# Kernel optimization log

Measured on AMD Instinct MI355X. Metric: run time of the kernel, lower is better.

Reference implementation:

```python
import jax, jax.numpy as jnp
import numpy as np

ANCHORS = jnp.array([[0.57273, 0.677385], [1.87446, 2.06253], [3.33843, 5.47434],
                     [7.88282, 3.52778], [9.77052, 9.16828]], dtype=jnp.float32)
IOU_THR = 0.6
SCALE_NOOBJ = 1.0
SCALE_OBJ = 5.0
DS = 32.0          # downsample_rate
EPS = 1e-7


def _iou_wh(w1, h1, w2, h2):
    # GetCenterAlignIouBetween: boxes aligned at centers -> IoU depends on w,h only
    inter = jnp.minimum(w1, w2) * jnp.minimum(h1, h2)
    return inter / (w1 * h1 + w2 * h2 - inter + EPS)


def setup_inputs() -> dict:
    B, W, H, A, C, M = 128, 19, 19, 5, 81, 24
    N = W * H
    key = jax.random.key(0)
    ks = jax.random.split(key, 8)
    ii, jj = jnp.meshgrid(jnp.arange(W), jnp.arange(H), indexing='ij')
    fm_cord = jnp.stack([jj, ii], -1).reshape(N, 2).astype(jnp.float32)  # (x=j, y=i)
    conf = jax.random.uniform(ks[0], (B, W, H, A, 1)) * 0.98 + 0.01      # valid BCE probs
    pred_xy = fm_cord.reshape(1, W, H, 1, 2) + jax.random.uniform(ks[1], (B, W, H, A, 2))
    pred_wh = jax.random.uniform(ks[2], (B, W, H, A, 2)) * 8.0 + 0.2     # fm units, >0
    cls_score = jax.random.normal(ks[3], (B, W, H, A, C))
    # distinct grid cells per image so sequential scatter == vectorized scatter
    cells = jax.vmap(lambda k: jax.random.choice(k, N, (M,), replace=False))(
        jax.random.split(ks[4], B))
    ci = cells // H
    cj = cells % H
    frac = jax.random.uniform(ks[5], (B, M, 2))
    x = (cj.astype(jnp.float32) + frac[..., 0]) * DS   # pixel coords
    y = (ci.astype(jnp.float32) + frac[..., 1]) * DS
    wh = jax.random.uniform(ks[6], (B, M, 2), minval=12.0, maxval=280.0)
    true_object = jnp.stack([x, y, wh[..., 0], wh[..., 1]], -1)          # [B,M,4] pixels
    labels = jax.random.randint(ks[7], (B, M), 0, C - 1)
    true_label = jax.nn.one_hot(labels, C, dtype=jnp.float32)            # [B,M,C]
    return dict(epoch=0, conf=conf, pred_xy=pred_xy, pred_wh=pred_wh,
                cls_score=cls_score, true_label=true_label,
                true_object=true_object, fm_cord=fm_cord)


def _yolo_loss(conf, pred_xy, pred_wh, cls_score, true_label, true_object, fm_cord):
    B, W, H, A, C = cls_score.shape
    N = W * H
    NA = N * A
    S = float(W)  # config.output_size

    # ---- target assignment (vectorized version of the python loops) ----
    obj = true_object / DS                               # fm units, [B,M,4]
    gx, gy, gw, gh = obj[..., 0], obj[..., 1], obj[..., 2], obj[..., 3]
    i = gy.astype(jnp.int32)                             # row index  (int() truncation)
    j = gx.astype(jnp.int32)                             # col index
    cell = i * H + j                                     # flat cell, [B,M]

    a_iou = _iou_wh(ANCHORS[None, None, :, 0], ANCHORS[None, None, :, 1],
                    gw[..., None], gh[..., None])        # [B,M,A]
    best = jnp.argmax(a_iou, axis=-1)                    # [B,M]
    is_best = best[..., None] == jnp.arange(A)[None, None, :]
    over = a_iou > IOU_THR

    bb = jnp.arange(B)[:, None]
    pwh = pred_wh.reshape(B, N, A, 2)[bb, cell]          # [B,M,A,2] gather at gt cells
    pwh_b = jnp.take_along_axis(pwh, best[..., None, None], axis=2)[:, :, 0]  # [B,M,2]
    iou_pg = _iou_wh(pwh_b[..., 0], pwh_b[..., 1], gw, gh)                    # [B,M]

    mask_val = jnp.where(is_best, 1.0, jnp.where(over, -1.0, 0.0))            # [B,M,A]
    sw = 2.0 - (gw / S) * (gh / S)                                            # [B,M]
    sw_val = jnp.where(is_best, sw[..., None], jnp.where(over, -1.0, 0.0))
    pgi_val = jnp.where(~is_best & over, 0.0, iou_pg[..., None])              # [B,M,A]
    bg = jax.nn.one_hot(C - 1, C, dtype=cls_score.dtype)
    ts_val = jnp.where((is_best | over)[..., None], true_label[:, :, None, :], bg)
    bbox_val = jnp.where(is_best[..., None], obj[:, :, None, :], 0.0)         # [B,M,A,4]

    obj_mask = jnp.zeros((B, N, A)).at[bb, cell].set(mask_val)
    scale_w = jnp.zeros((B, N, A)).at[bb, cell].set(sw_val)
    pgi = jnp.zeros((B, N, A)).at[bb, cell].set(pgi_val)
    true_score = jnp.zeros((B, N, A, C)).at[..., -1].set(1.0).at[bb, cell].set(ts_val)
    true_bbox = jnp.zeros((B, N, A, 4)).at[bb, cell].set(bbox_val)

    # ---- masked losses over flattened [B, W*H*A, ...] ----
    conf_f = conf.reshape(B, NA)
    om = obj_mask.reshape(B, NA)
    swf = scale_w.reshape(B, NA)
    pgif = pgi.reshape(B, NA)
    pxy = pred_xy.reshape(B, NA, 2)
    pwh_f = pred_wh.reshape(B, NA, 2)
    tb = true_bbox.reshape(B, NA, 4)
    ts = true_score.reshape(B, NA, C)
    cs = cls_score.reshape(B, NA, C)
    cord = jnp.repeat(fm_cord[:, None, :], A, axis=1).reshape(NA, 2)

    cp = jnp.clip(conf_f, EPS, 1.0 - EPS)
    noobj_loss = SCALE_NOOBJ * jnp.sum((om == 0) * (-jnp.log(1.0 - cp))) / B
    obj_loss = SCALE_OBJ * jnp.sum(
        (om == 1) * (-(pgif * jnp.log(cp) + (1.0 - pgif) * jnp.log(1.0 - cp)))) / B

    gt = (swf > 0).astype(conf_f.dtype)                  # [B,NA]
    w3 = (SCALE_OBJ * gt * swf)[..., None]
    xy_loss = jnp.sum(w3 * ((pxy - cord[None]) - (tb[..., :2] - cord[None])) ** 2) / B
    wh_loss = jnp.sum(w3 * (pwh_f - tb[..., 2:]) ** 2) / B

    # CE with soft targets, per position: [B,NA]
    ce = -jnp.sum(ts * jax.nn.log_softmax(cs, axis=-1), axis=-1)
    # original broadcasts mask [B,1,NA] * ce [B,NA] -> [B,B,NA] then .sum();
    # equivalent factored form: sum_n (sum_b1 mask) * (sum_b2 ce)
    score_loss = SCALE_OBJ * jnp.sum(gt.sum(0) * ce.sum(0)) / B

    total = noobj_loss + obj_loss + xy_loss + wh_loss + score_loss
    return total, noobj_loss, obj_loss, score_loss, xy_loss, wh_loss


def reference(epoch, conf, pred_xy, pred_wh, cls_score, true_label, true_object, fm_cord):
    return _yolo_loss(conf, pred_xy, pred_wh, cls_score,
                      true_label, true_object, fm_cord)
```

## Files before the change

kernel.cpp:

```cpp
#include <hip/hip_runtime.h>

#define Bsz 128
#define Wd 19
#define Hd 19
#define Ad 5
#define Cd 81
#define Md 24
#define Nd (Wd*Hd)
#define NAd (Nd*Ad)
#define TOTPOS (Bsz*NAd)
#define PPB 128
#define EPSF 1e-7f
#define IOU_THRF 0.6f

#define WS_FLOATS (4 + 2*NAd)

__global__ __launch_bounds__(64) void yolo_assign(
        const float* __restrict__ conf,
        const float* __restrict__ pred_xy,
        const float* __restrict__ pred_wh,
        const float* __restrict__ cls_score,
        const float* __restrict__ true_label,
        const float* __restrict__ true_object,
        float* __restrict__ ws) {
    int idx = blockIdx.x * 64 + threadIdx.x;
    const float AW[5] = {0.57273f, 1.87446f, 3.33843f, 7.88282f, 9.77052f};
    const float AH[5] = {0.677385f, 2.06253f, 5.47434f, 3.52778f, 9.16828f};
    int b = idx / Md;

    const float4 to = ((const float4*)true_object)[idx];
    const float inv_ds = 1.0f / 32.0f;
    float gx = to.x * inv_ds, gy = to.y * inv_ds;
    float gw = to.z * inv_ds, gh = to.w * inv_ds;
    int ci = (int)gy, cj = (int)gx;
    int cell = ci * Hd + cj;
    float garea = gw * gh;

    float best_iou = -1.0f; int best = 0; bool over[Ad];
    #pragma unroll
    for (int a = 0; a < Ad; a++) {
        float inter = fminf(AW[a], gw) * fminf(AH[a], gh);
        float iou = inter / (AW[a] * AH[a] + garea - inter + EPSF);
        over[a] = iou > IOU_THRF;
        if (iou > best_iou) { best_iou = iou; best = a; }
    }

    const float* tl = true_label + (size_t)idx * Cd;
    float labf = 0.0f;
    for (int c = 0; c < Cd; c++) labf += tl[c] * (float)c;
    int lab = (int)(labf + 0.5f);

    int base_bn = (b * Nd + cell) * Ad;
    float pwb = pred_wh[(size_t)(base_bn + best) * 2 + 0];
    float phb = pred_wh[(size_t)(base_bn + best) * 2 + 1];
    float inter = fminf(pwb, gw) * fminf(phb, gh);
    float iou_pg = inter / (pwb * phb + garea - inter + EPSF);
    float sw = 2.0f - (gw * (1.0f / 19.0f)) * (gh * (1.0f / 19.0f));

    float* gtsum = ws + 4;
    float* cesum = ws + 4 + NAd;

    float a0 = 0.f, a1 = 0.f, a2 = 0.f, a3 = 0.f;
    #pragma unroll
    for (int a = 0; a < Ad; a++) {
        bool isb = (a == best);
        if (!(isb || over[a])) continue;
        int pos = base_bn + a;
        int na  = cell * Ad + a;
        float cp = fminf(fmaxf(conf[pos], EPSF), 1.0f - EPSF);
        a0 += __logf(1.0f - cp);
        const float* cs = cls_score + (size_t)pos * Cd;
        atomicAdd(&cesum[na], cs[Cd - 1] - cs[lab]);
        if (isb) {
            atomicAdd(&gtsum[na], 1.0f);
            a1 += -(iou_pg * __logf(cp) + (1.0f - iou_pg) * __logf(1.0f - cp));
            float px = pred_xy[(size_t)pos * 2 + 0], py = pred_xy[(size_t)pos * 2 + 1];
            a2 += sw * ((px - gx) * (px - gx) + (py - gy) * (py - gy));
            float pwa = pred_wh[(size_t)pos * 2 + 0], pha = pred_wh[(size_t)pos * 2 + 1];
            a3 += sw * ((pwa - gw) * (pwa - gw) + (pha - gh) * (pha - gh));
        }
    }

    #pragma unroll
    for (int off = 32; off > 0; off >>= 1) {
        a0 += __shfl_down(a0, off, 64);
        a1 += __shfl_down(a1, off, 64);
        a2 += __shfl_down(a2, off, 64);
        a3 += __shfl_down(a3, off, 64);
    }
    if (threadIdx.x == 0) {
        atomicAdd(&ws[0], a0);
        atomicAdd(&ws[1], a1);
        atomicAdd(&ws[2], a2);
        atomicAdd(&ws[3], a3);
    }
}

__global__ __launch_bounds__(256) void yolo_sweep(
        const float* __restrict__ conf,
        const float* __restrict__ cls_score,
        float* __restrict__ ws) {
    __shared__ float ex[PPB * Cd];
    __shared__ float red[4];
    const int tid = threadIdx.x;
    const int bid = blockIdx.x;
    const int CHUNK4 = PPB * Cd / 4;

    const float4* g = (const float4*)(cls_score + (size_t)bid * (PPB * Cd));
    float4* l4 = (float4*)ex;
    for (int k = tid; k < CHUNK4; k += 256) {
        float4 v = g[k];
        v.x = __expf(v.x); v.y = __expf(v.y);
        v.z = __expf(v.z); v.w = __expf(v.w);
        l4[k] = v;
    }

    float noobj = 0.0f;
    if (tid < PPB) {
        float cp = fminf(fmaxf(conf[bid * PPB + tid], EPSF), 1.0f - EPSF);
        noobj = -__logf(1.0f - cp);
    }
    __syncthreads();

    int pos = tid >> 1, half = tid & 1;
    const float* base = ex + pos * Cd;
    float s = 0.0f;
    int c0 = half * 40, c1 = half ? Cd : 40;
    for (int c = c0; c < c1; c++) s += base[c];
    float S = s + __shfl_xor(s, 1, 64);
    if (half == 0) {
        float ce = __logf(S) - __logf(base[Cd - 1]);
        int na = (bid * PPB) % NAd + pos;
        if (na >= NAd) na -= NAd;
        atomicAdd(&ws[4 + NAd + na], ce);
    }

    #pragma unroll
    for (int off = 32; off > 0; off >>= 1) noobj += __shfl_down(noobj, off, 64);
    if ((tid & 63) == 0) red[tid >> 6] = noobj;
    __syncthreads();
    if (tid == 0) atomicAdd(&ws[0], red[0] + red[1] + red[2] + red[3]);
}

__global__ void yolo_finalize(const float* __restrict__ ws, float* __restrict__ out) {
    __shared__ float red[4];
    const float* gtsum = ws + 4;
    const float* cesum = ws + 4 + NAd;
    float s = 0.0f;
    for (int na = threadIdx.x; na < NAd; na += blockDim.x)
        s += gtsum[na] * cesum[na];
    #pragma unroll
    for (int off = 32; off > 0; off >>= 1) s += __shfl_down(s, off, 64);
    if ((threadIdx.x & 63) == 0) red[threadIdx.x >> 6] = s;
    __syncthreads();
    if (threadIdx.x == 0) {
        float tot = red[0] + red[1] + red[2] + red[3];
        const float invB = 1.0f / (float)Bsz;
        float noobj = 1.0f * ws[0] * invB;
        float obj   = 5.0f * ws[1] * invB;
        float xy    = 5.0f * ws[2] * invB;
        float wh    = 5.0f * ws[3] * invB;
        float score = 5.0f * tot  * invB;
        out[0] = noobj + obj + xy + wh + score;
        out[1] = noobj;
        out[2] = obj;
        out[3] = score;
        out[4] = xy;
        out[5] = wh;
    }
}

extern "C" void kernel_launch(void* const* d_in, const int* in_sizes, int n_in,
                              void* d_out, int out_size, void* d_ws, size_t ws_size,
                              hipStream_t stream) {
    const float* conf    = (const float*)d_in[1];
    const float* pred_xy = (const float*)d_in[2];
    const float* pred_wh = (const float*)d_in[3];
    const float* cls     = (const float*)d_in[4];
    const float* tlabel  = (const float*)d_in[5];
    const float* tobject = (const float*)d_in[6];
    float* ws  = (float*)d_ws;
    float* out = (float*)d_out;

    hipMemsetAsync(ws, 0, WS_FLOATS * sizeof(float), stream);

    yolo_assign<<<48, 64, 0, stream>>>(conf, pred_xy, pred_wh, cls, tlabel, tobject, ws);

    yolo_sweep<<<TOTPOS / PPB, 256, 0, stream>>>(conf, cls, ws);

    yolo_finalize<<<1, 256, 0, stream>>>(ws, out);
}
```

Before: 159.4 us.

## Replace per-position CE atomics with plain stores and reduce columns in finalize

The sweep kernel now handles 64 positions per block with four threads per position and applies exp while summing, instead of exponentiating during the shared-memory staging. It writes each per-position cross-entropy to its own workspace slot rather than issuing an atomicAdd into a per-anchor array. The finalize kernel, widened to 1024 threads, sums those values over the batch for each anchor slot. The assign kernel reads each label vector with a whole wavefront and runs after the sweep. Atomic contention goes away, but the workspace grows by one float per position and a single block must reduce all of them.

```diff
diff --git a/kernel.cpp b/kernel.cpp
--- a/kernel.cpp
+++ b/kernel.cpp
@@ -9,13 +9,16 @@
 #define Nd (Wd*Hd)
 #define NAd (Nd*Ad)
 #define TOTPOS (Bsz*NAd)
-#define PPB 128
+#define PPB 64
 #define EPSF 1e-7f
 #define IOU_THRF 0.6f
 
-#define WS_FLOATS (4 + 2*NAd)
-
-__global__ __launch_bounds__(64) void yolo_assign(
+#define OFF_GT   4
+#define OFF_CORR (4 + NAd)
+#define OFF_CE   4096
+#define MEMSET_FLOATS (4 + 2*NAd)
+
+__global__ __launch_bounds__(256) void yolo_assign(
         const float* __restrict__ conf,
         const float* __restrict__ pred_xy,
         const float* __restrict__ pred_wh,
@@ -23,76 +26,79 @@
         const float* __restrict__ true_label,
         const float* __restrict__ true_object,
         float* __restrict__ ws) {
-    int idx = blockIdx.x * 64 + threadIdx.x;
     const float AW[5] = {0.57273f, 1.87446f, 3.33843f, 7.88282f, 9.77052f};
     const float AH[5] = {0.677385f, 2.06253f, 5.47434f, 3.52778f, 9.16828f};
-    int b = idx / Md;
-
-    const float4 to = ((const float4*)true_object)[idx];
-    const float inv_ds = 1.0f / 32.0f;
-    float gx = to.x * inv_ds, gy = to.y * inv_ds;
-    float gw = to.z * inv_ds, gh = to.w * inv_ds;
-    int ci = (int)gy, cj = (int)gx;
-    int cell = ci * Hd + cj;
-    float garea = gw * gh;
-
-    float best_iou = -1.0f; int best = 0; bool over[Ad];
-    #pragma unroll
-    for (int a = 0; a < Ad; a++) {
-        float inter = fminf(AW[a], gw) * fminf(AH[a], gh);
-        float iou = inter / (AW[a] * AH[a] + garea - inter + EPSF);
-        over[a] = iou > IOU_THRF;
-        if (iou > best_iou) { best_iou = iou; best = a; }
-    }
-
-    const float* tl = true_label + (size_t)idx * Cd;
-    float labf = 0.0f;
-    for (int c = 0; c < Cd; c++) labf += tl[c] * (float)c;
-    int lab = (int)(labf + 0.5f);
-
-    int base_bn = (b * Nd + cell) * Ad;
-    float pwb = pred_wh[(size_t)(base_bn + best) * 2 + 0];
-    float phb = pred_wh[(size_t)(base_bn + best) * 2 + 1];
-    float inter = fminf(pwb, gw) * fminf(phb, gh);
-    float iou_pg = inter / (pwb * phb + garea - inter + EPSF);
-    float sw = 2.0f - (gw * (1.0f / 19.0f)) * (gh * (1.0f / 19.0f));
-
-    float* gtsum = ws + 4;
-    float* cesum = ws + 4 + NAd;
-
+    int wave = threadIdx.x >> 6, lane = threadIdx.x & 63;
     float a0 = 0.f, a1 = 0.f, a2 = 0.f, a3 = 0.f;
-    #pragma unroll
-    for (int a = 0; a < Ad; a++) {
-        bool isb = (a == best);
-        if (!(isb || over[a])) continue;
-        int pos = base_bn + a;
-        int na  = cell * Ad + a;
-        float cp = fminf(fmaxf(conf[pos], EPSF), 1.0f - EPSF);
-        a0 += __logf(1.0f - cp);
-        const float* cs = cls_score + (size_t)pos * Cd;
-        atomicAdd(&cesum[na], cs[Cd - 1] - cs[lab]);
-        if (isb) {
-            atomicAdd(&gtsum[na], 1.0f);
-            a1 += -(iou_pg * __logf(cp) + (1.0f - iou_pg) * __logf(1.0f - cp));
-            float px = pred_xy[(size_t)pos * 2 + 0], py = pred_xy[(size_t)pos * 2 + 1];
-            a2 += sw * ((px - gx) * (px - gx) + (py - gy) * (py - gy));
-            float pwa = pred_wh[(size_t)pos * 2 + 0], pha = pred_wh[(size_t)pos * 2 + 1];
-            a3 += sw * ((pwa - gw) * (pwa - gw) + (pha - gh) * (pha - gh));
+    float* gtsum = ws + OFF_GT;
+    float* corr  = ws + OFF_CORR;
+
+    int objBase = (blockIdx.x * 4 + wave) * 8;
+    for (int o = 0; o < 8; o++) {
+        int idx = objBase + o;
+        const float* tl = true_label + (size_t)idx * Cd;
+        float labf = tl[lane] * (float)lane;
+        if (lane < Cd - 64) labf += tl[64 + lane] * (float)(64 + lane);
+        #pragma unroll
+        for (int off = 32; off > 0; off >>= 1) labf += __shfl_down(labf, off, 64);
+
+        if (lane == 0) {
+            int lab = (int)(labf + 0.5f);
+            int b = idx / Md;
+            const float4 to = ((const float4*)true_object)[idx];
+            const float inv_ds = 1.0f / 32.0f;
+            float gx = to.x * inv_ds, gy = to.y * inv_ds;
+            float gw = to.z * inv_ds, gh = to.w * inv_ds;
+            int ci = (int)gy, cj = (int)gx;
+            int cell = ci * Hd + cj;
+            float garea = gw * gh;
+
+            float best_iou = -1.0f; int best = 0; bool over[Ad];
+            #pragma unroll
+            for (int a = 0; a < Ad; a++) {
+                float inter = fminf(AW[a], gw) * fminf(AH[a], gh);
+                float iou = inter / (AW[a] * AH[a] + garea - inter + EPSF);
+                over[a] = iou > IOU_THRF;
+                if (iou > best_iou) { best_iou = iou; best = a; }
+            }
+
+            int base_bn = (b * Nd + cell) * Ad;
+            float pwb = pred_wh[(size_t)(base_bn + best) * 2 + 0];
+            float phb = pred_wh[(size_t)(base_bn + best) * 2 + 1];
+            float inter = fminf(pwb, gw) * fminf(phb, gh);
+            float iou_pg = inter / (pwb * phb + garea - inter + EPSF);
+            float sw = 2.0f - (gw * (1.0f / 19.0f)) * (gh * (1.0f / 19.0f));
+
+            #pragma unroll
+            for (int a = 0; a < Ad; a++) {
+                bool isb = (a == best);
+                if (!(isb || over[a])) continue;
+                int pos = base_bn + a;
+                int na  = cell * Ad + a;
+                float cp = fminf(fmaxf(conf[pos], EPSF), 1.0f - EPSF);
+                a0 += __logf(1.0f - cp);
+                const float* cs = cls_score + (size_t)pos * Cd;
+                atomicAdd(&corr[na], cs[Cd - 1] - cs[lab]);
+                if (isb) {
+                    atomicAdd(&gtsum[na], 1.0f);
+                    a1 += -(iou_pg * __logf(cp) + (1.0f - iou_pg) * __logf(1.0f - cp));
+                    float px = pred_xy[(size_t)pos * 2 + 0], py = pred_xy[(size_t)pos * 2 + 1];
+                    a2 += sw * ((px - gx) * (px - gx) + (py - gy) * (py - gy));
+                    float pwa = pred_wh[(size_t)pos * 2 + 0], pha = pred_wh[(size_t)pos * 2 + 1];
+                    a3 += sw * ((pwa - gw) * (pwa - gw) + (pha - gh) * (pha - gh));
+                }
+            }
         }
     }
 
-    #pragma unroll
-    for (int off = 32; off > 0; off >>= 1) {
-        a0 += __shfl_down(a0, off, 64);
-        a1 += __shfl_down(a1, off, 64);
-        a2 += __shfl_down(a2, off, 64);
-        a3 += __shfl_down(a3, off, 64);
-    }
+    __shared__ float red[4][4];
+    if (lane == 0) { red[wave][0] = a0; red[wave][1] = a1; red[wave][2] = a2; red[wave][3] = a3; }
+    __syncthreads();
     if (threadIdx.x == 0) {
-        atomicAdd(&ws[0], a0);
-        atomicAdd(&ws[1], a1);
-        atomicAdd(&ws[2], a2);
-        atomicAdd(&ws[3], a3);
+        atomicAdd(&ws[0], red[0][0] + red[1][0] + red[2][0] + red[3][0]);
+        atomicAdd(&ws[1], red[0][1] + red[1][1] + red[2][1] + red[3][1]);
+        atomicAdd(&ws[2], red[0][2] + red[1][2] + red[2][2] + red[3][2]);
+        atomicAdd(&ws[3], red[0][3] + red[1][3] + red[2][3] + red[3][3]);
     }
 }
 
@@ -101,60 +107,75 @@
         const float* __restrict__ cls_score,
         float* __restrict__ ws) {
     __shared__ float ex[PPB * Cd];
-    __shared__ float red[4];
-    const int tid = threadIdx.x;
-    const int bid = blockIdx.x;
-    const int CHUNK4 = PPB * Cd / 4;
+    const int tid = threadIdx.x, bid = blockIdx.x;
+    const int wave = tid >> 6, lane = tid & 63;
+    const int base = wave * 324;
 
     const float4* g = (const float4*)(cls_score + (size_t)bid * (PPB * Cd));
     float4* l4 = (float4*)ex;
-    for (int k = tid; k < CHUNK4; k += 256) {
-        float4 v = g[k];
-        v.x = __expf(v.x); v.y = __expf(v.y);
-        v.z = __expf(v.z); v.w = __expf(v.w);
-        l4[k] = v;
-    }
-
-    float noobj = 0.0f;
+
+    float4 r0 = g[base + 0 * 64 + lane];
+    float4 r1 = g[base + 1 * 64 + lane];
+    float4 r2 = g[base + 2 * 64 + lane];
+    float4 r3 = g[base + 3 * 64 + lane];
+    float4 r4 = g[base + 4 * 64 + lane];
+    float4 r5 = g[base + 260 + lane];
+
+    float nb = 0.0f;
     if (tid < PPB) {
         float cp = fminf(fmaxf(conf[bid * PPB + tid], EPSF), 1.0f - EPSF);
-        noobj = -__logf(1.0f - cp);
-    }
+        nb = -__logf(1.0f - cp);
+    }
+
+    l4[base + 0 * 64 + lane] = r0;
+    l4[base + 1 * 64 + lane] = r1;
+    l4[base + 2 * 64 + lane] = r2;
+    l4[base + 3 * 64 + lane] = r3;
+    l4[base + 4 * 64 + lane] = r4;
+    l4[base + 260 + lane] = r5;
     __syncthreads();
 
-    int pos = tid >> 1, half = tid & 1;
-    const float* base = ex + pos * Cd;
+    int pos = tid >> 2, h = tid & 3;
+    const float* p = ex + pos * Cd;
+    int c0 = h * 20, c1 = (h == 3) ? Cd : c0 + 20;
     float s = 0.0f;
-    int c0 = half * 40, c1 = half ? Cd : 40;
-    for (int c = c0; c < c1; c++) s += base[c];
-    float S = s + __shfl_xor(s, 1, 64);
-    if (half == 0) {
-        float ce = __logf(S) - __logf(base[Cd - 1]);
-        int na = (bid * PPB) % NAd + pos;
-        if (na >= NAd) na -= NAd;
-        atomicAdd(&ws[4 + NAd + na], ce);
-    }
-
-    #pragma unroll
-    for (int off = 32; off > 0; off >>= 1) noobj += __shfl_down(noobj, off, 64);
-    if ((tid & 63) == 0) red[tid >> 6] = noobj;
-    __syncthreads();
-    if (tid == 0) atomicAdd(&ws[0], red[0] + red[1] + red[2] + red[3]);
-}
-
-__global__ void yolo_finalize(const float* __restrict__ ws, float* __restrict__ out) {
-    __shared__ float red[4];
-    const float* gtsum = ws + 4;
-    const float* cesum = ws + 4 + NAd;
+    for (int c = c0; c < c1; c++) s += __expf(p[c]);
+    s += __shfl_xor(s, 1, 64);
+    s += __shfl_xor(s, 2, 64);
+    if (h == 0) {
+        float ce = __logf(s) - p[Cd - 1];
+        ws[OFF_CE + bid * PPB + pos] = ce;
+    }
+
+    if (wave == 0) {
+        #pragma unroll
+        for (int off = 32; off > 0; off >>= 1) nb += __shfl_down(nb, off, 64);
+        if (lane == 0) atomicAdd(&ws[0], nb);
+    }
+}
+
+__global__ __launch_bounds__(1024) void yolo_finalize(
+        const float* __restrict__ ws, float* __restrict__ out) {
+    __shared__ float red[16];
+    const float* gtsum = ws + OFF_GT;
+    const float* corr  = ws + OFF_CORR;
+    const float* cef   = ws + OFF_CE;
     float s = 0.0f;
-    for (int na = threadIdx.x; na < NAd; na += blockDim.x)
-        s += gtsum[na] * cesum[na];
+    for (int na = threadIdx.x; na < NAd; na += 1024) {
+        float sum = corr[na];
+        const float* col = cef + na;
+        #pragma unroll 4
+        for (int b = 0; b < Bsz; b++) sum += col[(size_t)b * NAd];
+        s += gtsum[na] * sum;
+    }
     #pragma unroll
     for (int off = 32; off > 0; off >>= 1) s += __shfl_down(s, off, 64);
     if ((threadIdx.x & 63) == 0) red[threadIdx.x >> 6] = s;
     __syncthreads();
     if (threadIdx.x == 0) {
-        float tot = red[0] + red[1] + red[2] + red[3];
+        float tot = 0.f;
+        #pragma unroll
+        for (int i = 0; i < 16; i++) tot += red[i];
         const float invB = 1.0f / (float)Bsz;
         float noobj = 1.0f * ws[0] * invB;
         float obj   = 5.0f * ws[1] * invB;
@@ -182,11 +203,11 @@
     float* ws  = (float*)d_ws;
     float* out = (float*)d_out;
 
-    hipMemsetAsync(ws, 0, WS_FLOATS * sizeof(float), stream);
-
-    yolo_assign<<<48, 64, 0, stream>>>(conf, pred_xy, pred_wh, cls, tlabel, tobject, ws);
+    hipMemsetAsync(ws, 0, MEMSET_FLOATS * sizeof(float), stream);
 
     yolo_sweep<<<TOTPOS / PPB, 256, 0, stream>>>(conf, cls, ws);
 
-    yolo_finalize<<<1, 256, 0, stream>>>(ws, out);
-}
+    yolo_assign<<<96, 256, 0, stream>>>(conf, pred_xy, pred_wh, cls, tlabel, tobject, ws);
+
+    yolo_finalize<<<1, 1024, 0, stream>>>(ws, out);
+}
```

New measurement: 210.3 us. 31.9% more time.

## Merge assignment into sweep and final kernels with per-wave row blocks

Applied to the files above, without the earlier changes.

Removes the separate assignment kernel. Label decoding moves into the sweep kernel as extra one-wave blocks, and the target-assignment work moves into a single 1024-thread final kernel that accumulates into shared-memory atomics. The sweep now launches one 64-lane block per 16 rows, so many more blocks share the load, and each block writes its no-object partial to its own slot instead of issuing global atomics. The cost is that assignment runs serially inside one block at the end, which could become the critical path.

```diff
diff --git a/kernel.cpp b/kernel.cpp
--- a/kernel.cpp
+++ b/kernel.cpp
@@ -1,166 +1,194 @@
 #include <hip/hip_runtime.h>
 
 #define Bsz 128
-#define Wd 19
-#define Hd 19
-#define Ad 5
 #define Cd 81
 #define Md 24
-#define Nd (Wd*Hd)
-#define NAd (Nd*Ad)
-#define TOTPOS (Bsz*NAd)
-#define PPB 128
+#define Nd 361
+#define NAd 1805
+#define TOTPOS 231040
+#define RPW 16
+#define NW_CLS (TOTPOS/RPW)
+#define NOBJ (Bsz*Md)
+#define NW_LAB (NOBJ/RPW)
 #define EPSF 1e-7f
 #define IOU_THRF 0.6f
 
-#define WS_FLOATS (4 + 2*NAd)
-
-__global__ __launch_bounds__(64) void yolo_assign(
+#define OFF_CESUM 0
+#define OFF_NOOBJ 2048
+#define OFF_LAB   17408
+
+__global__ __launch_bounds__(64) void yolo_sweep(
+        const float* __restrict__ conf,
+        const float* __restrict__ cls_score,
+        const float* __restrict__ true_label,
+        float* __restrict__ ws) {
+    __shared__ float ex[RPW * Cd];
+    const int bid = blockIdx.x;
+    const int lane = threadIdx.x;
+    const bool is_cls = bid < NW_CLS;
+
+    const float* src = is_cls ? (cls_score + (size_t)bid * (RPW * Cd))
+                              : (true_label + (size_t)(bid - NW_CLS) * (RPW * Cd));
+    const float4* g = (const float4*)src;
+    float4 r0 = g[0 * 64 + lane];
+    float4 r1 = g[1 * 64 + lane];
+    float4 r2 = g[2 * 64 + lane];
+    float4 r3 = g[3 * 64 + lane];
+    float4 r4 = g[4 * 64 + lane];
+    float4 r5 = g[260 + lane];
+
+    float nb = 0.0f;
+    if (is_cls) {
+        if (lane < RPW) {
+            float cp = fminf(fmaxf(conf[bid * RPW + lane], EPSF), 1.0f - EPSF);
+            nb = -__logf(1.0f - cp);
+        }
+        r0.x = __expf(r0.x); r0.y = __expf(r0.y); r0.z = __expf(r0.z); r0.w = __expf(r0.w);
+        r1.x = __expf(r1.x); r1.y = __expf(r1.y); r1.z = __expf(r1.z); r1.w = __expf(r1.w);
+        r2.x = __expf(r2.x); r2.y = __expf(r2.y); r2.z = __expf(r2.z); r2.w = __expf(r2.w);
+        r3.x = __expf(r3.x); r3.y = __expf(r3.y); r3.z = __expf(r3.z); r3.w = __expf(r3.w);
+        r4.x = __expf(r4.x); r4.y = __expf(r4.y); r4.z = __expf(r4.z); r4.w = __expf(r4.w);
+        r5.x = __expf(r5.x); r5.y = __expf(r5.y); r5.z = __expf(r5.z); r5.w = __expf(r5.w);
+    }
+    float4* l4 = (float4*)ex;
+    l4[0 * 64 + lane] = r0;
+    l4[1 * 64 + lane] = r1;
+    l4[2 * 64 + lane] = r2;
+    l4[3 * 64 + lane] = r3;
+    l4[4 * 64 + lane] = r4;
+    l4[260 + lane] = r5;
+    __syncthreads();
+
+    const int r = lane >> 2, h = lane & 3;
+    const float* p = ex + r * Cd;
+    float s = 0.0f;
+    #pragma unroll
+    for (int j = 0; j < 21; j++) {
+        int c = h * 21 + j;
+        int cc = c < 81 ? c : 80;
+        float w = (c < 81) ? (is_cls ? 1.0f : (float)c) : 0.0f;
+        s += p[cc] * w;
+    }
+    s += __shfl_xor(s, 1, 64);
+    s += __shfl_xor(s, 2, 64);
+
+    if (h == 0) {
+        int row = bid * RPW + r;
+        if (is_cls) {
+            float ce = __logf(s) - __logf(p[80]);
+            int na = row % NAd;
+            atomicAdd(&ws[OFF_CESUM + na], ce);
+        } else {
+            ws[OFF_LAB + ((bid - NW_CLS) * RPW + r)] = s;
+        }
+    }
+    if (is_cls) {
+        #pragma unroll
+        for (int off = 32; off > 0; off >>= 1) nb += __shfl_xor(nb, off, 64);
+        if (lane == 0) ws[OFF_NOOBJ + bid] = nb;
+    }
+}
+
+__global__ __launch_bounds__(1024) void yolo_final(
         const float* __restrict__ conf,
         const float* __restrict__ pred_xy,
         const float* __restrict__ pred_wh,
         const float* __restrict__ cls_score,
-        const float* __restrict__ true_label,
         const float* __restrict__ true_object,
-        float* __restrict__ ws) {
-    int idx = blockIdx.x * 64 + threadIdx.x;
+        const float* __restrict__ ws,
+        float* __restrict__ out) {
+    __shared__ float gt[NAd];
+    __shared__ float corr[NAd];
+    __shared__ float red[6][16];
     const float AW[5] = {0.57273f, 1.87446f, 3.33843f, 7.88282f, 9.77052f};
     const float AH[5] = {0.677385f, 2.06253f, 5.47434f, 3.52778f, 9.16828f};
-    int b = idx / Md;
-
-    const float4 to = ((const float4*)true_object)[idx];
-    const float inv_ds = 1.0f / 32.0f;
-    float gx = to.x * inv_ds, gy = to.y * inv_ds;
-    float gw = to.z * inv_ds, gh = to.w * inv_ds;
-    int ci = (int)gy, cj = (int)gx;
-    int cell = ci * Hd + cj;
-    float garea = gw * gh;
-
-    float best_iou = -1.0f; int best = 0; bool over[Ad];
-    #pragma unroll
-    for (int a = 0; a < Ad; a++) {
-        float inter = fminf(AW[a], gw) * fminf(AH[a], gh);
-        float iou = inter / (AW[a] * AH[a] + garea - inter + EPSF);
-        over[a] = iou > IOU_THRF;
-        if (iou > best_iou) { best_iou = iou; best = a; }
-    }
-
-    const float* tl = true_label + (size_t)idx * Cd;
-    float labf = 0.0f;
-    for (int c = 0; c < Cd; c++) labf += tl[c] * (float)c;
-    int lab = (int)(labf + 0.5f);
-
-    int base_bn = (b * Nd + cell) * Ad;
-    float pwb = pred_wh[(size_t)(base_bn + best) * 2 + 0];
-    float phb = pred_wh[(size_t)(base_bn + best) * 2 + 1];
-    float inter = fminf(pwb, gw) * fminf(phb, gh);
-    float iou_pg = inter / (pwb * phb + garea - inter + EPSF);
-    float sw = 2.0f - (gw * (1.0f / 19.0f)) * (gh * (1.0f / 19.0f));
-
-    float* gtsum = ws + 4;
-    float* cesum = ws + 4 + NAd;
+    const int tid = threadIdx.x;
+
+    for (int i = tid; i < NAd; i += 1024) { gt[i] = 0.0f; corr[i] = 0.0f; }
+    __syncthreads();
 
     float a0 = 0.f, a1 = 0.f, a2 = 0.f, a3 = 0.f;
     #pragma unroll
-    for (int a = 0; a < Ad; a++) {
-        bool isb = (a == best);
-        if (!(isb || over[a])) continue;
-        int pos = base_bn + a;
-        int na  = cell * Ad + a;
-        float cp = fminf(fmaxf(conf[pos], EPSF), 1.0f - EPSF);
-        a0 += __logf(1.0f - cp);
-        const float* cs = cls_score + (size_t)pos * Cd;
-        atomicAdd(&cesum[na], cs[Cd - 1] - cs[lab]);
-        if (isb) {
-            atomicAdd(&gtsum[na], 1.0f);
-            a1 += -(iou_pg * __logf(cp) + (1.0f - iou_pg) * __logf(1.0f - cp));
-            float px = pred_xy[(size_t)pos * 2 + 0], py = pred_xy[(size_t)pos * 2 + 1];
-            a2 += sw * ((px - gx) * (px - gx) + (py - gy) * (py - gy));
-            float pwa = pred_wh[(size_t)pos * 2 + 0], pha = pred_wh[(size_t)pos * 2 + 1];
-            a3 += sw * ((pwa - gw) * (pwa - gw) + (pha - gh) * (pha - gh));
-        }
-    }
-
+    for (int o = 0; o < 3; o++) {
+        int idx = tid + o * 1024;
+        int lab = (int)(ws[OFF_LAB + idx] + 0.5f);
+        int b = idx / Md;
+        const float4 to = ((const float4*)true_object)[idx];
+        const float inv_ds = 1.0f / 32.0f;
+        float gx = to.x * inv_ds, gy = to.y * inv_ds;
+        float gw = to.z * inv_ds, gh = to.w * inv_ds;
+        int ci = (int)gy, cj = (int)gx;
+        int cell = ci * 19 + cj;
+        float garea = gw * gh;
+
+        float best_iou = -1.0f; int best = 0; bool over[5];
+        #pragma unroll
+        for (int a = 0; a < 5; a++) {
+            float inter = fminf(AW[a], gw) * fminf(AH[a], gh);
+            float iou = inter / (AW[a] * AH[a] + garea - inter + EPSF);
+            over[a] = iou > IOU_THRF;
+            if (iou > best_iou) { best_iou = iou; best = a; }
+        }
+
+        int base_bn = (b * Nd + cell) * 5;
+        float pwb = pred_wh[(size_t)(base_bn + best) * 2 + 0];
+        float phb = pred_wh[(size_t)(base_bn + best) * 2 + 1];
+        float inter = fminf(pwb, gw) * fminf(phb, gh);
+        float iou_pg = inter / (pwb * phb + garea - inter + EPSF);
+        float sw = 2.0f - (gw * (1.0f / 19.0f)) * (gh * (1.0f / 19.0f));
+
+        #pragma unroll
+        for (int a = 0; a < 5; a++) {
+            bool isb = (a == best);
+            if (!(isb || over[a])) continue;
+            int pos = base_bn + a;
+            int na  = cell * 5 + a;
+            float cp = fminf(fmaxf(conf[pos], EPSF), 1.0f - EPSF);
+            a0 += __logf(1.0f - cp);
+            const float* cs = cls_score + (size_t)pos * Cd;
+            atomicAdd(&corr[na], cs[Cd - 1] - cs[lab]);
+            if (isb) {
+                atomicAdd(&gt[na], 1.0f);
+                a1 += -(iou_pg * __logf(cp) + (1.0f - iou_pg) * __logf(1.0f - cp));
+                float px = pred_xy[(size_t)pos * 2 + 0], py = pred_xy[(size_t)pos * 2 + 1];
+                a2 += sw * ((px - gx) * (px - gx) + (py - gy) * (py - gy));
+                float pwa = pred_wh[(size_t)pos * 2 + 0], pha = pred_wh[(size_t)pos * 2 + 1];
+                a3 += sw * ((pwa - gw) * (pwa - gw) + (pha - gh) * (pha - gh));
+            }
+        }
+    }
+    __syncthreads();
+
+    float nsum = 0.0f;
+    for (int i = tid; i < NW_CLS; i += 1024) nsum += ws[OFF_NOOBJ + i];
+    float ssum = 0.0f;
+    for (int na = tid; na < NAd; na += 1024)
+        ssum += gt[na] * (corr[na] + ws[OFF_CESUM + na]);
+
+    float v[6] = {a0, a1, a2, a3, nsum, ssum};
     #pragma unroll
-    for (int off = 32; off > 0; off >>= 1) {
-        a0 += __shfl_down(a0, off, 64);
-        a1 += __shfl_down(a1, off, 64);
-        a2 += __shfl_down(a2, off, 64);
-        a3 += __shfl_down(a3, off, 64);
-    }
-    if (threadIdx.x == 0) {
-        atomicAdd(&ws[0], a0);
-        atomicAdd(&ws[1], a1);
-        atomicAdd(&ws[2], a2);
-        atomicAdd(&ws[3], a3);
-    }
-}
-
-__global__ __launch_bounds__(256) void yolo_sweep(
-        const float* __restrict__ conf,
-        const float* __restrict__ cls_score,
-        float* __restrict__ ws) {
-    __shared__ float ex[PPB * Cd];
-    __shared__ float red[4];
-    const int tid = threadIdx.x;
-    const int bid = blockIdx.x;
-    const int CHUNK4 = PPB * Cd / 4;
-
-    const float4* g = (const float4*)(cls_score + (size_t)bid * (PPB * Cd));
-    float4* l4 = (float4*)ex;
-    for (int k = tid; k < CHUNK4; k += 256) {
-        float4 v = g[k];
-        v.x = __expf(v.x); v.y = __expf(v.y);
-        v.z = __expf(v.z); v.w = __expf(v.w);
-        l4[k] = v;
-    }
-
-    float noobj = 0.0f;
-    if (tid < PPB) {
-        float cp = fminf(fmaxf(conf[bid * PPB + tid], EPSF), 1.0f - EPSF);
-        noobj = -__logf(1.0f - cp);
-    }
-    __syncthreads();
-
-    int pos = tid >> 1, half = tid & 1;
-    const float* base = ex + pos * Cd;
-    float s = 0.0f;
-    int c0 = half * 40, c1 = half ? Cd : 40;
-    for (int c = c0; c < c1; c++) s += base[c];
-    float S = s + __shfl_xor(s, 1, 64);
-    if (half == 0) {
-        float ce = __logf(S) - __logf(base[Cd - 1]);
-        int na = (bid * PPB) % NAd + pos;
-        if (na >= NAd) na -= NAd;
-        atomicAdd(&ws[4 + NAd + na], ce);
-    }
-
-    #pragma unroll
-    for (int off = 32; off > 0; off >>= 1) noobj += __shfl_down(noobj, off, 64);
-    if ((tid & 63) == 0) red[tid >> 6] = noobj;
-    __syncthreads();
-    if (tid == 0) atomicAdd(&ws[0], red[0] + red[1] + red[2] + red[3]);
-}
-
-__global__ void yolo_finalize(const float* __restrict__ ws, float* __restrict__ out) {
-    __shared__ float red[4];
-    const float* gtsum = ws + 4;
-    const float* cesum = ws + 4 + NAd;
-    float s = 0.0f;
-    for (int na = threadIdx.x; na < NAd; na += blockDim.x)
-        s += gtsum[na] * cesum[na];
-    #pragma unroll
-    for (int off = 32; off > 0; off >>= 1) s += __shfl_down(s, off, 64);
-    if ((threadIdx.x & 63) == 0) red[threadIdx.x >> 6] = s;
-    __syncthreads();
-    if (threadIdx.x == 0) {
-        float tot = red[0] + red[1] + red[2] + red[3];
+    for (int k = 0; k < 6; k++) {
+        float x = v[k];
+        #pragma unroll
+        for (int off = 32; off > 0; off >>= 1) x += __shfl_xor(x, off, 64);
+        if ((tid & 63) == 0) red[k][tid >> 6] = x;
+    }
+    __syncthreads();
+    if (tid == 0) {
+        float t[6];
+        #pragma unroll
+        for (int k = 0; k < 6; k++) {
+            float x = 0.f;
+            #pragma unroll
+            for (int w = 0; w < 16; w++) x += red[k][w];
+            t[k] = x;
+        }
         const float invB = 1.0f / (float)Bsz;
-        float noobj = 1.0f * ws[0] * invB;
-        float obj   = 5.0f * ws[1] * invB;
-        float xy    = 5.0f * ws[2] * invB;
-        float wh    = 5.0f * ws[3] * invB;
-        float score = 5.0f * tot  * invB;
+        float noobj = 1.0f * (t[4] + t[0]) * invB;
+        float obj   = 5.0f * t[1] * invB;
+        float xy    = 5.0f * t[2] * invB;
+        float wh    = 5.0f * t[3] * invB;
+        float score = 5.0f * t[5] * invB;
         out[0] = noobj + obj + xy + wh + score;
         out[1] = noobj;
         out[2] = obj;
@@ -182,11 +210,9 @@
     float* ws  = (float*)d_ws;
     float* out = (float*)d_out;
 
-    hipMemsetAsync(ws, 0, WS_FLOATS * sizeof(float), stream);
-
-    yolo_assign<<<48, 64, 0, stream>>>(conf, pred_xy, pred_wh, cls, tlabel, tobject, ws);
-
-    yolo_sweep<<<TOTPOS / PPB, 256, 0, stream>>>(conf, cls, ws);
-
-    yolo_finalize<<<1, 256, 0, stream>>>(ws, out);
+    hipMemsetAsync(ws + OFF_CESUM, 0, NAd * sizeof(float), stream);
+
+    yolo_sweep<<<NW_CLS + NW_LAB, 64, 0, stream>>>(conf, cls, tlabel, ws);
+
+    yolo_final<<<1, 1024, 0, stream>>>(conf, pred_xy, pred_wh, cls, tobject, ws, out);
 }
```

Measured after the change: 165.4 us. 1.04x slower.
